# Optimization experiments

Measured on AMD Instinct MI355X. Metric: run time of the kernel, lower is better.

The kernel has to match this reference:

```python
import jax, jax.numpy as jnp
import numpy as np

# Llama-3-8B-like attention, prefill over B sequences of length S (flattened tokens)
D = 4096      # hidden_size
N = 32        # num query heads
K = 8         # num KV heads (GQA)
H = 128       # head_dim (== head_dim_original, already a multiple of 128 so no padding)
B = 4         # sequences in the ragged batch
S = 1024      # tokens per sequence
T = B * S     # total flattened tokens
ROPE_THETA = 10000.0


def _apply_rope(x, positions, head_dim, theta):
    # x: [T, n_heads, H]; positions: [T] int
    inv_freq = 1.0 / (theta ** (jnp.arange(0, head_dim, 2, dtype=jnp.float32) / head_dim))
    freqs = positions.astype(jnp.float32)[:, None] * inv_freq[None, :]  # [T, H/2]
    emb = jnp.concatenate([freqs, freqs], axis=-1)                       # [T, H]
    cos = jnp.cos(emb)[:, None, :].astype(x.dtype)
    sin = jnp.sin(emb)[:, None, :].astype(x.dtype)
    x1, x2 = jnp.split(x, 2, axis=-1)
    rotated = jnp.concatenate([-x2, x1], axis=-1)
    return x * cos + rotated * sin


def setup_inputs() -> dict:
    key = jax.random.key(0)
    ks = jax.random.split(key, 5)
    x = jax.random.normal(ks[0], (T, D), dtype=jnp.float32)
    # positions restart per sequence (ragged prefill metadata)
    input_positions = (jnp.arange(T, dtype=jnp.int32) % S)
    w_scale = 0.02
    Wq = jax.random.normal(ks[1], (D, N, H), dtype=jnp.float32) * w_scale
    Wk = jax.random.normal(ks[2], (D, K, H), dtype=jnp.float32) * w_scale
    Wv = jax.random.normal(ks[3], (D, K, H), dtype=jnp.float32) * w_scale
    Wo = jax.random.normal(ks[4], (N, H, D), dtype=jnp.float32) * w_scale
    return {"x": x, "input_positions": input_positions,
            "Wq": Wq, "Wk": Wk, "Wv": Wv, "Wo": Wo}


def reference(x, input_positions, Wq, Wk, Wv, Wo):
    # QKV projections (flattened tokens)
    q = jnp.einsum('td,dnh->tnh', x, Wq)   # [T, N, H]
    k = jnp.einsum('td,dkh->tkh', x, Wk)   # [T, K, H]
    v = jnp.einsum('td,dkh->tkh', x, Wv)   # [T, K, H]
    q = _apply_rope(q, input_positions, H, ROPE_THETA)
    k = _apply_rope(k, input_positions, H, ROPE_THETA)

    # Ragged causal attention: per-sequence causal SDPA with GQA head grouping.
    G = N // K  # query heads per KV head
    qb = q.reshape(B, S, K, G, H)
    kb = k.reshape(B, S, K, H)
    vb = v.reshape(B, S, K, H)
    scale = jnp.asarray(H, q.dtype) ** -0.5  # head_dim_original ** -0.5
    scores = jnp.einsum('bqkgh,bskh->bkgqs', qb, kb) * scale  # [B,K,G,S,S]
    causal = jnp.tril(jnp.ones((S, S), dtype=bool))
    scores = jnp.where(causal, scores, jnp.finfo(scores.dtype).min)
    probs = jax.nn.softmax(scores, axis=-1)
    out = jnp.einsum('bkgqs,bskh->bqkgh', probs, vb).reshape(T, N, H)

    # Output projection
    o = jnp.einsum('tnh,nhd->td', out, Wo)  # [T, D]
    return o
```

## Files before the change

### kernel.cpp

```cpp
#include <hip/hip_runtime.h>
#include <cstdint>


typedef unsigned short u16;
typedef short bf16x8 __attribute__((ext_vector_type(8)));
typedef float f32x4 __attribute__((ext_vector_type(4)));

#define L2E 1.44269504088896340736f

static __device__ __forceinline__ u16 f2bf(float f) {
  union { float f; unsigned u; } v; v.f = f;
  unsigned r = (v.u + 0x7fffu + ((v.u >> 16) & 1u)) >> 16;
  return (u16)r;
}
static __device__ __forceinline__ float bf2f(u16 h) {
  union { unsigned u; float f; } v; v.u = ((unsigned)h) << 16;
  return v.f;
}

typedef __attribute__((address_space(1))) const unsigned int gas_u32;
typedef __attribute__((address_space(3))) unsigned int las_u32;
static __device__ __forceinline__ void glds16(const void* g, const void* l) {
  __builtin_amdgcn_global_load_lds((gas_u32*)(uintptr_t)g,
                                   (las_u32*)(unsigned)(uintptr_t)l, 16, 0, 0);
}

__global__ __launch_bounds__(256) void cvt_kernel(const float4* __restrict__ in,
                                                  uint2* __restrict__ out, int n4) {
  int i = blockIdx.x * 256 + threadIdx.x;
  if (i < n4) {
    float4 v = in[i];
    uint2 r;
    r.x = (unsigned)f2bf(v.x) | ((unsigned)f2bf(v.y) << 16);
    r.y = (unsigned)f2bf(v.z) | ((unsigned)f2bf(v.w) << 16);
    out[i] = r;
  }
}

__global__ __launch_bounds__(256) void tcvt_kernel(const float* __restrict__ in,
                                                   u16* __restrict__ out, int R, int C) {
  __shared__ float tile[32][33];
  int tx = threadIdx.x, ty = threadIdx.y;
  int r0 = blockIdx.y * 32, c0 = blockIdx.x * 32;
#pragma unroll
  for (int j = 0; j < 4; ++j)
    tile[ty + j * 8][tx] = in[(size_t)(r0 + ty + j * 8) * C + c0 + tx];
  __syncthreads();
#pragma unroll
  for (int j = 0; j < 4; ++j)
    out[(size_t)(c0 + ty + j * 8) * R + r0 + tx] = f2bf(tile[tx][ty + j * 8]);
}

template <int BF16OUT>
__global__ __launch_bounds__(512, 2) void gemm_nt8(const u16* __restrict__ A,
                                                   const u16* __restrict__ Bm,
                                                   void* __restrict__ Cp,
                                                   int M, int N, int Kd) {
  __shared__ u16 Als[2][2][8192];
  __shared__ u16 Bls[2][2][8192];
  const int tid = threadIdx.x;
  const int w = tid >> 6, lane = tid & 63;
  const int ln15 = lane & 15, quad = lane >> 4;
  const int wm = w & 1, wn = w >> 1;

  const int nbm = M >> 8;
  const int nwg = nbm * (N >> 8);
  const int cpx = nwg >> 3;
  const int bid = blockIdx.x;
  const int swz = (bid & 7) * cpx + (bid >> 3);
  const int bm = swz & (nbm - 1);
  const int bn = swz / nbm;
  const int m0 = bm << 8, n0 = bn << 8;

  const int nt = Kd >> 6;

  const int srow = lane >> 2;
  const int schk = ((lane & 3) ^ ((lane >> 3) & 3)) << 3;
  const u16* aSrc = A + (size_t)(m0 + w * 32 + srow) * Kd + schk;
  const u16* bSrc = Bm + (size_t)(n0 + w * 32 + srow) * Kd + schk;
  const int ldsb = w * 1024;

  const int rswz = (quad ^ ((ln15 >> 1) & 3)) << 3;
  const int aoff = (wm * 128 + ln15) * 32 + rswz;
  const int boff = (wn * 64 + ln15) * 32 + rswz;

  f32x4 acc[8][4];
#pragma unroll
  for (int i = 0; i < 8; ++i)
#pragma unroll
    for (int j = 0; j < 4; ++j) acc[i][j] = f32x4{0.f, 0.f, 0.f, 0.f};
  bf16x8 af[8];

#define STA(kt, buf, ks)                                          \
  do {                                                            \
    int kc_ = (kt) < nt ? (kt) : nt - 1;                          \
    const u16* s_ = aSrc + (size_t)kc_ * 64 + (ks) * 32;          \
    glds16(s_, &Als[buf][ks][ldsb]);                              \
    glds16(s_ + (size_t)16 * Kd, &Als[buf][ks][ldsb + 512]);      \
  } while (0)
#define STB(kt, buf, ks)                                          \
  do {                                                            \
    int kc_ = (kt) < nt ? (kt) : nt - 1;                          \
    const u16* s_ = bSrc + (size_t)kc_ * 64 + (ks) * 32;          \
    glds16(s_, &Bls[buf][ks][ldsb]);                              \
    glds16(s_ + (size_t)16 * Kd, &Bls[buf][ks][ldsb + 512]);      \
  } while (0)

#define PHASE(buf, ks, nh, STAGE, VM)                                              \
  do {                                                                             \
    if ((nh) == 0) {                                                               \
      _Pragma("unroll") for (int m_ = 0; m_ < 8; ++m_)                             \
          af[m_] = *(const bf16x8*)&Als[buf][ks][aoff + m_ * 512];                 \
    }                                                                              \
    bf16x8 b0_ = *(const bf16x8*)&Bls[buf][ks][boff + (nh) * 1024];                \
    bf16x8 b1_ = *(const bf16x8*)&Bls[buf][ks][boff + (nh) * 1024 + 512];          \
    STAGE;                                                                         \
    __builtin_amdgcn_s_barrier();                                                  \
    __builtin_amdgcn_s_setprio(1);                                                 \
    _Pragma("unroll") for (int m_ = 0; m_ < 8; ++m_) {                             \
      acc[m_][2 * (nh)] =                                                          \
          __builtin_amdgcn_mfma_f32_16x16x32_bf16(af[m_], b0_, acc[m_][2 * (nh)],  \
                                                  0, 0, 0);                        \
      acc[m_][2 * (nh) + 1] = __builtin_amdgcn_mfma_f32_16x16x32_bf16(             \
          af[m_], b1_, acc[m_][2 * (nh) + 1], 0, 0, 0);                            \
    }                                                                              \
    __builtin_amdgcn_s_setprio(0);                                                 \
    if (VM) asm volatile("s_waitcnt vmcnt(6)" ::: "memory");                       \
    __builtin_amdgcn_s_barrier();                                                  \
    __builtin_amdgcn_sched_barrier(0);                                             \
  } while (0)

  STA(0, 0, 0); STB(0, 0, 0); STA(0, 0, 1); STB(0, 0, 1);
  STA(1, 1, 0); STB(1, 1, 0); STA(1, 1, 1);
  asm volatile("s_waitcnt vmcnt(6)" ::: "memory");
  __builtin_amdgcn_s_barrier();
  __builtin_amdgcn_sched_barrier(0);

  const int iters = nt >> 1;
  for (int i = 0; i < iters; ++i) {
    const int t = 2 * i;
    PHASE(0, 0, 0, STB(t + 1, 1, 1), 0);
    PHASE(0, 0, 1, STA(t + 2, 0, 0), 0);
    PHASE(0, 1, 0, STB(t + 2, 0, 0), 0);
    PHASE(0, 1, 1, STA(t + 2, 0, 1), 1);
    PHASE(1, 0, 0, STB(t + 2, 0, 1), 0);
    PHASE(1, 0, 1, STA(t + 3, 1, 0), 0);
    PHASE(1, 1, 0, STB(t + 3, 1, 0), 0);
    PHASE(1, 1, 1, STA(t + 3, 1, 1), 1);
  }
#undef PHASE
#undef STA
#undef STB

  const int crow = m0 + wm * 128 + quad * 4;
  const int ccol = n0 + wn * 64 + ln15;
#pragma unroll
  for (int m = 0; m < 8; ++m)
#pragma unroll
    for (int j = 0; j < 4; ++j)
#pragma unroll
      for (int r = 0; r < 4; ++r) {
        float v = acc[m][j][r];
        if (BF16OUT)
          ((u16*)Cp)[(size_t)(crow + m * 16 + r) * N + ccol + j * 16] = f2bf(v);
        else
          ((float*)Cp)[(size_t)(crow + m * 16 + r) * N + ccol + j * 16] = v;
      }
}

__global__ __launch_bounds__(256) void rope_kernel(u16* __restrict__ qkv,
                                                   const int* __restrict__ pos, int total) {
  int idx = blockIdx.x * 256 + threadIdx.x;
  if (idx >= total) return;
  int t = idx / 2560;
  int rem = idx - t * 2560;
  int head = rem >> 6;
  int i = rem & 63;
  float p = (float)pos[t];
  float inv = exp2f(-0.20751874963942190927f * (float)i);
  float f = p * inv;
  float s, c;
  sincosf(f, &s, &c);
  int colbase = (head < 32) ? head * 128 : (4096 + (head - 32) * 128);
  u16* base = qkv + (size_t)t * 6144 + colbase;
  float x1 = bf2f(base[i]), x2 = bf2f(base[i + 64]);
  float o1 = x1 * c - x2 * s;
  float o2 = x2 * c + x1 * s;
  if (head < 32) { o1 *= 0.08838834764831845f; o2 *= 0.08838834764831845f; }
  base[i] = f2bf(o1);
  base[i + 64] = f2bf(o2);
}

__global__ __launch_bounds__(256, 3) void attn_kernel(const u16* __restrict__ qkv,
                                                      u16* __restrict__ outp) {
  __shared__ u16 Klds[64 * 128];
  __shared__ u16 Vtlds[128 * 72];
  __shared__ u16 Plds[4 * 16 * 72];

  const int bx = blockIdx.x;
  const int qb = 15 - (bx & 15);
  const int n = (bx >> 4) & 31;
  const int b = bx >> 9;
  const int kh = n >> 2;

  const int tid = threadIdx.x;
  const int w = tid >> 6;
  const int lane = tid & 63;
  const int ln15 = lane & 15;
  const int quad = lane >> 4;

  const int ldq = 6144;
  const int seq0 = b << 10;
  const int q0 = seq0 + qb * 64;

  const u16* Qg = qkv + n * 128;
  const u16* Kg = qkv + 4096 + kh * 128;
  const u16* Vg = qkv + 5120 + kh * 128;

  bf16x8 qf[4];
  {
    const u16* qrow = Qg + (size_t)(q0 + w * 16 + ln15) * ldq + quad * 8;
#pragma unroll
    for (int ks = 0; ks < 4; ++ks) qf[ks] = *(const bf16x8*)(qrow + ks * 32);
  }

  f32x4 o[8];
#pragma unroll
  for (int i = 0; i < 8; ++i) o[i] = f32x4{0.f, 0.f, 0.f, 0.f};
  float m_r[4] = {-INFINITY, -INFINITY, -INFINITY, -INFINITY};
  float l_r[4] = {0.f, 0.f, 0.f, 0.f};

  const int krow = w * 4 + (lane >> 4);
  const int kcol = (((lane & 15) ^ (krow & 7)) << 3);

  const int vs0 = (lane & 31) * 2;
  const int vhb = w * 32 + (lane >> 5) * 16;

  for (int kt = 0; kt <= qb; ++kt) {
    __syncthreads();
    {
      const u16* kbase = Kg + (size_t)(seq0 + kt * 64 + krow) * ldq + kcol;
#pragma unroll
      for (int q = 0; q < 4; ++q)
        glds16(kbase + (size_t)q * 16 * ldq, &Klds[(q * 16 + w * 4) * 128]);
    }
    {
      const u16* v0 = Vg + (size_t)(seq0 + kt * 64 + vs0) * ldq + vhb;
      union { uint4 v[2]; u16 s[16]; } ra, rb;
      ra.v[0] = *(const uint4*)v0;
      ra.v[1] = *(const uint4*)(v0 + 8);
      rb.v[0] = *(const uint4*)(v0 + ldq);
      rb.v[1] = *(const uint4*)(v0 + ldq + 8);
#pragma unroll
      for (int j = 0; j < 16; ++j) {
        unsigned pk = (unsigned)ra.s[j] | ((unsigned)rb.s[j] << 16);
        *(unsigned*)&Vtlds[(vhb + j) * 72 + vs0] = pk;
      }
    }
    __syncthreads();

    f32x4 sfr[4];
#pragma unroll
    for (int c = 0; c < 4; ++c) {
      f32x4 acc = f32x4{0.f, 0.f, 0.f, 0.f};
#pragma unroll
      for (int ks = 0; ks < 4; ++ks) {
        int rr = c * 16 + ln15;
        int ph = (ks * 4 + quad) ^ (rr & 7);
        bf16x8 kf = *(const bf16x8*)&Klds[rr * 128 + ph * 8];
        acc = __builtin_amdgcn_mfma_f32_16x16x32_bf16(qf[ks], kf, acc, 0, 0, 0);
      }
      sfr[c] = acc;
    }

    if (kt == qb) {
#pragma unroll
      for (int c = 0; c < 4; ++c) {
        int col = c * 16 + ln15;
#pragma unroll
        for (int r = 0; r < 4; ++r)
          if (col > w * 16 + quad * 4 + r) sfr[c][r] = -INFINITY;
      }
    }

    float alpha[4];
#pragma unroll
    for (int r = 0; r < 4; ++r) {
      float mx = fmaxf(fmaxf(sfr[0][r], sfr[1][r]), fmaxf(sfr[2][r], sfr[3][r]));
      mx = fmaxf(mx, __shfl_xor(mx, 1));
      mx = fmaxf(mx, __shfl_xor(mx, 2));
      mx = fmaxf(mx, __shfl_xor(mx, 4));
      mx = fmaxf(mx, __shfl_xor(mx, 8));
      float mnew = fmaxf(m_r[r], mx);
      alpha[r] = exp2f((m_r[r] - mnew) * L2E);
      m_r[r] = mnew;
      float rs = 0.f;
#pragma unroll
      for (int c = 0; c < 4; ++c) {
        float pv = exp2f((sfr[c][r] - mnew) * L2E);
        sfr[c][r] = pv;
        rs += pv;
      }
      rs += __shfl_xor(rs, 1);
      rs += __shfl_xor(rs, 2);
      rs += __shfl_xor(rs, 4);
      rs += __shfl_xor(rs, 8);
      l_r[r] = alpha[r] * l_r[r] + rs;
    }

#pragma unroll
    for (int ht = 0; ht < 8; ++ht)
#pragma unroll
      for (int r = 0; r < 4; ++r) o[ht][r] *= alpha[r];

#pragma unroll
    for (int c = 0; c < 4; ++c)
#pragma unroll
      for (int r = 0; r < 4; ++r)
        Plds[w * 1152 + (quad * 4 + r) * 72 + c * 16 + ln15] = f2bf(sfr[c][r]);

    asm volatile("s_waitcnt lgkmcnt(0)" ::: "memory");

    bf16x8 pf[2];
#pragma unroll
    for (int ks = 0; ks < 2; ++ks)
      pf[ks] = *(const bf16x8*)&Plds[w * 1152 + ln15 * 72 + ks * 32 + quad * 8];
#pragma unroll
    for (int ht = 0; ht < 8; ++ht) {
#pragma unroll
      for (int ks = 0; ks < 2; ++ks) {
        bf16x8 vf = *(const bf16x8*)&Vtlds[(ht * 16 + ln15) * 72 + ks * 32 + quad * 8];
        o[ht] = __builtin_amdgcn_mfma_f32_16x16x32_bf16(pf[ks], vf, o[ht], 0, 0, 0);
      }
    }
  }

#pragma unroll
  for (int r = 0; r < 4; ++r) l_r[r] = 1.f / l_r[r];
#pragma unroll
  for (int ht = 0; ht < 8; ++ht)
#pragma unroll
    for (int r = 0; r < 4; ++r)
      outp[(size_t)(q0 + w * 16 + quad * 4 + r) * 4096 + n * 128 + ht * 16 + ln15] =
          f2bf(o[ht][r] * l_r[r]);
}

extern "C" void kernel_launch(void* const* d_in, const int* in_sizes, int n_in,
                              void* d_out, int out_size, void* d_ws, size_t ws_size,
                              hipStream_t stream) {
  const float* x = (const float*)d_in[0];
  const int* posi = (const int*)d_in[1];
  const float* Wq = (const float*)d_in[2];
  const float* Wk = (const float*)d_in[3];
  const float* Wv = (const float*)d_in[4];
  const float* Wo = (const float*)d_in[5];
  float* out = (float*)d_out;
  char* ws = (char*)d_ws;

  u16* xb = (u16*)(ws);
  u16* Wt = (u16*)(ws + 33554432);
  u16* WoT = (u16*)(ws + 83886080);
  u16* qkv = (u16*)(ws + 117440512);
  u16* attn = xb;

  cvt_kernel<<<16384, 256, 0, stream>>>((const float4*)x, (uint2*)xb, 4194304);
  tcvt_kernel<<<dim3(128, 128), dim3(32, 8), 0, stream>>>(Wq, Wt, 4096, 4096);
  tcvt_kernel<<<dim3(32, 128), dim3(32, 8), 0, stream>>>(Wk, Wt + (size_t)4096 * 4096, 4096, 1024);
  tcvt_kernel<<<dim3(32, 128), dim3(32, 8), 0, stream>>>(Wv, Wt + (size_t)5120 * 4096, 4096, 1024);
  tcvt_kernel<<<dim3(128, 128), dim3(32, 8), 0, stream>>>(Wo, WoT, 4096, 4096);

  gemm_nt8<1><<<dim3(384), 512, 0, stream>>>(xb, Wt, qkv, 4096, 6144, 4096);
  rope_kernel<<<40960, 256, 0, stream>>>(qkv, posi, 10485760);
  attn_kernel<<<2048, 256, 0, stream>>>(qkv, attn);
  gemm_nt8<0><<<dim3(256), 512, 0, stream>>>(attn, WoT, out, 4096, 4096, 4096);
}
```

Before: 782.5 us.

## Use inline-asm LDS reads, rope table, V prefetch, lazy softmax rescale

The GEMM's LDS fragment loads become inline ds_read_b128 with immediate offsets and an explicit lgkmcnt wait. RoPE now reads cos/sin from a precomputed table built by a new small kernel that overwrites the start of the xb workspace after the QKV GEMM has consumed it. The table is indexed by position, which assumes positions are below 1024. The attention kernel prefetches the next V tile into registers while computing the current one, and skips rescaling the output accumulator unless the running max grows by more than a threshold. That lazy rescale trades some headroom in the exponentials for fewer multiplies.

Measured after the change: 750.3 us. 4.1% less time.

```diff
diff --git a/kernel.cpp b/kernel.cpp
--- a/kernel.cpp
+++ b/kernel.cpp
@@ -83,6 +83,8 @@
   const int rswz = (quad ^ ((ln15 >> 1) & 3)) << 3;
   const int aoff = (wm * 128 + ln15) * 32 + rswz;
   const int boff = (wn * 64 + ln15) * 32 + rswz;
+  const unsigned aAddr = (unsigned)(uintptr_t)&Als[0][0][aoff];
+  const unsigned bAddr = (unsigned)(uintptr_t)&Bls[0][0][boff];
 
   f32x4 acc[8][4];
 #pragma unroll
@@ -90,6 +92,9 @@
 #pragma unroll
     for (int j = 0; j < 4; ++j) acc[i][j] = f32x4{0.f, 0.f, 0.f, 0.f};
   bf16x8 af[8];
+
+#define DSR(dst, addr, off) \
+  asm volatile("ds_read_b128 %0, %1 offset:%2" : "=v"(dst) : "v"(addr), "i"(off))
 
 #define STA(kt, buf, ks)                                          \
   do {                                                            \
@@ -109,13 +114,22 @@
 #define PHASE(buf, ks, nh, STAGE, VM)                                              \
   do {                                                                             \
     if ((nh) == 0) {                                                               \
-      _Pragma("unroll") for (int m_ = 0; m_ < 8; ++m_)                             \
-          af[m_] = *(const bf16x8*)&Als[buf][ks][aoff + m_ * 512];                 \
+      DSR(af[0], aAddr, (buf)*32768 + (ks)*16384 + 0 * 1024);                      \
+      DSR(af[1], aAddr, (buf)*32768 + (ks)*16384 + 1 * 1024);                      \
+      DSR(af[2], aAddr, (buf)*32768 + (ks)*16384 + 2 * 1024);                      \
+      DSR(af[3], aAddr, (buf)*32768 + (ks)*16384 + 3 * 1024);                      \
+      DSR(af[4], aAddr, (buf)*32768 + (ks)*16384 + 4 * 1024);                      \
+      DSR(af[5], aAddr, (buf)*32768 + (ks)*16384 + 5 * 1024);                      \
+      DSR(af[6], aAddr, (buf)*32768 + (ks)*16384 + 6 * 1024);                      \
+      DSR(af[7], aAddr, (buf)*32768 + (ks)*16384 + 7 * 1024);                      \
     }                                                                              \
-    bf16x8 b0_ = *(const bf16x8*)&Bls[buf][ks][boff + (nh) * 1024];                \
-    bf16x8 b1_ = *(const bf16x8*)&Bls[buf][ks][boff + (nh) * 1024 + 512];          \
+    bf16x8 b0_, b1_;                                                               \
+    DSR(b0_, bAddr, (buf)*32768 + (ks)*16384 + (nh)*2048);                         \
+    DSR(b1_, bAddr, (buf)*32768 + (ks)*16384 + (nh)*2048 + 1024);                  \
     STAGE;                                                                         \
     __builtin_amdgcn_s_barrier();                                                  \
+    asm volatile("s_waitcnt lgkmcnt(0)" ::: "memory");                             \
+    __builtin_amdgcn_sched_barrier(0);                                             \
     __builtin_amdgcn_s_setprio(1);                                                 \
     _Pragma("unroll") for (int m_ = 0; m_ < 8; ++m_) {                             \
       acc[m_][2 * (nh)] =                                                          \
@@ -151,6 +165,7 @@
 #undef PHASE
 #undef STA
 #undef STB
+#undef DSR
 
   const int crow = m0 + wm * 128 + quad * 4;
   const int ccol = n0 + wn * 64 + ln15;
@@ -168,19 +183,28 @@
       }
 }
 
+__global__ __launch_bounds__(256) void ropetab_kernel(float2* __restrict__ tab) {
+  int idx = blockIdx.x * 256 + threadIdx.x;
+  int i = idx & 63;
+  float inv = exp2f(-0.20751874963942190927f * (float)i);
+  float f = (float)(idx >> 6) * inv;
+  float s, c;
+  sincosf(f, &s, &c);
+  tab[idx] = make_float2(c, s);
+}
+
 __global__ __launch_bounds__(256) void rope_kernel(u16* __restrict__ qkv,
-                                                   const int* __restrict__ pos, int total) {
+                                                   const int* __restrict__ pos,
+                                                   const float2* __restrict__ tab,
+                                                   int total) {
   int idx = blockIdx.x * 256 + threadIdx.x;
   if (idx >= total) return;
   int t = idx / 2560;
   int rem = idx - t * 2560;
   int head = rem >> 6;
   int i = rem & 63;
-  float p = (float)pos[t];
-  float inv = exp2f(-0.20751874963942190927f * (float)i);
-  float f = p * inv;
-  float s, c;
-  sincosf(f, &s, &c);
+  float2 cs = tab[(pos[t] << 6) | i];
+  float c = cs.x, s = cs.y;
   int colbase = (head < 32) ? head * 128 : (4096 + (head - 32) * 128);
   u16* base = qkv + (size_t)t * 6144 + colbase;
   float x1 = bf2f(base[i]), x2 = bf2f(base[i + 64]);
@@ -236,6 +260,16 @@
   const int vs0 = (lane & 31) * 2;
   const int vhb = w * 32 + (lane >> 5) * 16;
 
+  union V16 { uint4 v[2]; u16 s[16]; };
+  V16 ra, rb;
+  {
+    const u16* v0 = Vg + (size_t)(seq0 + vs0) * ldq + vhb;
+    ra.v[0] = *(const uint4*)v0;
+    ra.v[1] = *(const uint4*)(v0 + 8);
+    rb.v[0] = *(const uint4*)(v0 + ldq);
+    rb.v[1] = *(const uint4*)(v0 + ldq + 8);
+  }
+
   for (int kt = 0; kt <= qb; ++kt) {
     __syncthreads();
     {
@@ -245,19 +279,21 @@
         glds16(kbase + (size_t)q * 16 * ldq, &Klds[(q * 16 + w * 4) * 128]);
     }
     {
-      const u16* v0 = Vg + (size_t)(seq0 + kt * 64 + vs0) * ldq + vhb;
-      union { uint4 v[2]; u16 s[16]; } ra, rb;
+#pragma unroll
+      for (int j = 0; j < 16; ++j) {
+        unsigned pk = (unsigned)ra.s[j] | ((unsigned)rb.s[j] << 16);
+        *(unsigned*)&Vtlds[(vhb + j) * 72 + vs0] = pk;
+      }
+    }
+    __syncthreads();
+
+    if (kt < qb) {
+      const u16* v0 = Vg + (size_t)(seq0 + (kt + 1) * 64 + vs0) * ldq + vhb;
       ra.v[0] = *(const uint4*)v0;
       ra.v[1] = *(const uint4*)(v0 + 8);
       rb.v[0] = *(const uint4*)(v0 + ldq);
       rb.v[1] = *(const uint4*)(v0 + ldq + 8);
-#pragma unroll
-      for (int j = 0; j < 16; ++j) {
-        unsigned pk = (unsigned)ra.s[j] | ((unsigned)rb.s[j] << 16);
-        *(unsigned*)&Vtlds[(vhb + j) * 72 + vs0] = pk;
-      }
-    }
-    __syncthreads();
+    }
 
     f32x4 sfr[4];
 #pragma unroll
@@ -283,21 +319,35 @@
       }
     }
 
-    float alpha[4];
+    float mx[4];
 #pragma unroll
     for (int r = 0; r < 4; ++r) {
-      float mx = fmaxf(fmaxf(sfr[0][r], sfr[1][r]), fmaxf(sfr[2][r], sfr[3][r]));
-      mx = fmaxf(mx, __shfl_xor(mx, 1));
-      mx = fmaxf(mx, __shfl_xor(mx, 2));
-      mx = fmaxf(mx, __shfl_xor(mx, 4));
-      mx = fmaxf(mx, __shfl_xor(mx, 8));
-      float mnew = fmaxf(m_r[r], mx);
-      alpha[r] = exp2f((m_r[r] - mnew) * L2E);
-      m_r[r] = mnew;
+      float m0 = fmaxf(fmaxf(sfr[0][r], sfr[1][r]), fmaxf(sfr[2][r], sfr[3][r]));
+      m0 = fmaxf(m0, __shfl_xor(m0, 1));
+      m0 = fmaxf(m0, __shfl_xor(m0, 2));
+      m0 = fmaxf(m0, __shfl_xor(m0, 4));
+      m0 = fmaxf(m0, __shfl_xor(m0, 8));
+      mx[r] = m0;
+    }
+    float ex = fmaxf(fmaxf(mx[0] - m_r[0], mx[1] - m_r[1]),
+                     fmaxf(mx[2] - m_r[2], mx[3] - m_r[3]));
+    if (!__all(ex <= 8.f)) {
+#pragma unroll
+      for (int r = 0; r < 4; ++r) {
+        float mnew = fmaxf(m_r[r], mx[r]);
+        float al = exp2f((m_r[r] - mnew) * L2E);
+        m_r[r] = mnew;
+        l_r[r] *= al;
+#pragma unroll
+        for (int ht = 0; ht < 8; ++ht) o[ht][r] *= al;
+      }
+    }
+#pragma unroll
+    for (int r = 0; r < 4; ++r) {
       float rs = 0.f;
 #pragma unroll
       for (int c = 0; c < 4; ++c) {
-        float pv = exp2f((sfr[c][r] - mnew) * L2E);
+        float pv = exp2f((sfr[c][r] - m_r[r]) * L2E);
         sfr[c][r] = pv;
         rs += pv;
       }
@@ -305,13 +355,8 @@
       rs += __shfl_xor(rs, 2);
       rs += __shfl_xor(rs, 4);
       rs += __shfl_xor(rs, 8);
-      l_r[r] = alpha[r] * l_r[r] + rs;
-    }
-
-#pragma unroll
-    for (int ht = 0; ht < 8; ++ht)
-#pragma unroll
-      for (int r = 0; r < 4; ++r) o[ht][r] *= alpha[r];
+      l_r[r] += rs;
+    }
 
 #pragma unroll
     for (int c = 0; c < 4; ++c)
@@ -362,6 +407,7 @@
   u16* WoT = (u16*)(ws + 83886080);
   u16* qkv = (u16*)(ws + 117440512);
   u16* attn = xb;
+  float2* rtab = (float2*)ws;
 
   cvt_kernel<<<16384, 256, 0, stream>>>((const float4*)x, (uint2*)xb, 4194304);
   tcvt_kernel<<<dim3(128, 128), dim3(32, 8), 0, stream>>>(Wq, Wt, 4096, 4096);
@@ -370,7 +416,8 @@
   tcvt_kernel<<<dim3(128, 128), dim3(32, 8), 0, stream>>>(Wo, WoT, 4096, 4096);
 
   gemm_nt8<1><<<dim3(384), 512, 0, stream>>>(xb, Wt, qkv, 4096, 6144, 4096);
-  rope_kernel<<<40960, 256, 0, stream>>>(qkv, posi, 10485760);
+  ropetab_kernel<<<256, 256, 0, stream>>>(rtab);
+  rope_kernel<<<40960, 256, 0, stream>>>(qkv, posi, rtab, 10485760);
   attn_kernel<<<2048, 256, 0, stream>>>(qkv, attn);
   gemm_nt8<0><<<dim3(256), 512, 0, stream>>>(attn, WoT, out, 4096, 4096, 4096);
 }
```
